# Performance work log

Hardware: AMD Instinct MI355X
Metric: run time of the kernel (lower is better)

Reference implementation:

```python
import jax, jax.numpy as jnp
import numpy as np

EPS = 1e-12  # torch F.normalize default eps


def _l2norm(x):
    n = jnp.sqrt(jnp.sum(x * x, axis=-1, keepdims=True))
    return x / jnp.maximum(n, EPS)


def setup_inputs() -> dict:
    key = jax.random.key(0)
    ks = jax.random.split(key, 8)
    B, T, V = 4, 2048, 512
    C, H, NB = 512, 4, 64
    return {
        "x": jax.random.normal(ks[0], (B, T, V), dtype=jnp.float32),
        "basis": jax.random.normal(ks[1], (V, 2 * NB), dtype=jnp.float32),
        "shared_q_w": jax.random.normal(ks[2], (V, C), dtype=jnp.float32) * 0.02,
        "shared_k_w": jax.random.normal(ks[3], (V, C), dtype=jnp.float32) * 0.02,
        "v_coeffs": jax.random.normal(ks[4], (C, 2 * NB), dtype=jnp.float32) * 0.02,
        "o_coeffs": jax.random.normal(ks[5], (C, 2 * NB), dtype=jnp.float32) * 0.02,
        "decay_logits": jnp.linspace(1.0, 5.0, H, dtype=jnp.float32),
        "out_scale": jnp.float32(0.1),
    }


def reference(x, basis, shared_q_w, shared_k_w, v_coeffs, o_coeffs, decay_logits, out_scale):
    B, T, V = x.shape
    H = decay_logits.shape[0]
    C = shared_q_w.shape[1]
    D = C // H

    v_w = basis @ v_coeffs.T  # [V, C]
    o_w = basis @ o_coeffs.T  # [V, C]

    q = _l2norm(x @ shared_q_w)  # [B, T, C]
    k = _l2norm(x @ shared_k_w)
    v = x @ v_w

    # [B, H, T, D]
    q = q.reshape(B, T, H, D).transpose(0, 2, 1, 3)
    k = k.reshape(B, T, H, D).transpose(0, 2, 1, 3)
    v = v.reshape(B, T, H, D).transpose(0, 2, 1, 3)

    scores = jnp.einsum("bhqd,bhkd->bhqk", q, k)  # [B, H, T, T]

    decay = jax.nn.sigmoid(decay_logits)  # [H]
    pos = jnp.arange(T)
    diff = pos[None, :] - pos[:, None]  # diff[i, j] = j - i
    mask = (diff > 0).astype(scores.dtype)  # [T, T]
    expo = jnp.clip(diff.astype(jnp.float32) - 1.0, 0.0, None)  # [T, T]
    decay_w = (decay[:, None, None] ** expo[None]) * mask[None]  # [H, T, T]

    scores = scores * decay_w[None].astype(scores.dtype)
    retrieved = jnp.einsum("bhqk,bhkd->bhqd", scores, v)  # [B, H, T, D]
    retrieved = retrieved.transpose(0, 2, 1, 3).reshape(B, T, C)
    return retrieved @ o_w.T * out_scale  # [B, T, V]
```

## Files before the change

### kernel.cpp

```cpp
#include <hip/hip_runtime.h>
#include <hip/hip_bf16.h>

#define BB 4
#define TT 2048
#define VV 512
#define CC 512
#define HH 4
#define DD 128
#define NB2 128
#define NROWS (BB*TT)
#define QC 64
#define NCH (TT/QC)
#define SST 66
#define EPS 1e-12f

typedef __attribute__((ext_vector_type(8))) short bf16x8;
typedef __attribute__((ext_vector_type(4))) float f32x4;
typedef unsigned short u16;

__device__ __forceinline__ void gl_lds16(const void* g, void* l) {
    __builtin_amdgcn_global_load_lds(
        (const __attribute__((address_space(1))) unsigned int*)g,
        (__attribute__((address_space(3))) unsigned int*)l, 16, 0, 0);
}
__device__ __forceinline__ u16 f2bu(float x) {
    __hip_bfloat16 h = __float2bfloat16(x);
    return *reinterpret_cast<u16*>(&h);
}
__device__ __forceinline__ float bu2f(u16 u) {
    __hip_bfloat16 h = *reinterpret_cast<__hip_bfloat16*>(&u);
    return __bfloat162float(h);
}
__device__ __forceinline__ uint4 pack8(float4 a, float4 b, float s) {
    u16 h[8] = {f2bu(a.x * s), f2bu(a.y * s), f2bu(a.z * s), f2bu(a.w * s),
                f2bu(b.x * s), f2bu(b.y * s), f2bu(b.z * s), f2bu(b.w * s)};
    return *(uint4*)h;
}

#define P2_CVT 4096
#define P2_TR  512
#define P2_Z   16
#define P2_WG  32
__global__ __launch_bounds__(256) void prep_all2(
    const float* __restrict__ x, const float* __restrict__ qw,
    const float* __restrict__ kw, const float* __restrict__ basis,
    const float* __restrict__ v_coeffs, const float* __restrict__ o_coeffs,
    const float* __restrict__ out_scale,
    u16* __restrict__ xb, u16* __restrict__ wq, u16* __restrict__ wk,
    u16* __restrict__ v_wT, u16* __restrict__ o_ws, float* __restrict__ norms)
{
    __shared__ __align__(16) union {
        float tile[32][33];
        struct { u16 A[4096]; u16 B[4096]; } w;
    } sm;
    const int bi = blockIdx.x, t = threadIdx.x;
    if (bi < P2_CVT) {
        int i = bi * 256 + t;
        float4 v = ((const float4*)x)[i];
        u16 h[4] = {f2bu(v.x), f2bu(v.y), f2bu(v.z), f2bu(v.w)};
        ((uint2*)xb)[i] = *(uint2*)h;
    } else if (bi < P2_CVT + P2_TR) {
        int id = bi - P2_CVT;
        const int z = id >> 8; id &= 255;
        const float* in = z ? kw : qw;
        u16* outT = z ? wk : wq;
        const int bx = (id & 15) * 32, by = (id >> 4) * 32;
        const int tx = t & 31, ty = t >> 5;
        #pragma unroll
        for (int r = 0; r < 32; r += 8)
            sm.tile[ty + r][tx] = in[(size_t)(by + ty + r) * CC + bx + tx];
        __syncthreads();
        #pragma unroll
        for (int r = 0; r < 32; r += 8)
            outT[(size_t)(bx + ty + r) * VV + by + tx] = f2bu(sm.tile[tx][ty + r]);
    } else if (bi < P2_CVT + P2_TR + P2_Z) {
        int idx = (bi - P2_CVT - P2_TR) * 256 + t;
        ((float4*)norms)[idx] = make_float4(0.f, 0.f, 0.f, 0.f);
    } else {
        int id = bi - (P2_CVT + P2_TR + P2_Z);
        const int sec = id >> 4, rem = id & 15;
        const int m0 = (rem >> 2) * 128, n0 = (rem & 3) * 128;
        const float* Af = sec ? basis : v_coeffs;
        const float* Bf = sec ? o_coeffs : basis;
        u16* Cp = sec ? o_ws : v_wT;
        const float scB = sec ? out_scale[0] : 1.f;
        const int wave = t >> 6, lane = t & 63;
        const int qq = lane >> 4, l16 = lane & 15;
        const int wm = (wave >> 1) * 64, wn = (wave & 1) * 64;
        const int s0 = wave * 128 + lane, s1 = s0 + 64;
        const int r0 = s0 >> 2, c0 = ((s0 & 3) - (r0 >> 1)) & 3;
        const int r1 = s1 >> 2, c1 = ((s1 & 3) - (r1 >> 1)) & 3;
        f32x4 acc[4][4];
        #pragma unroll
        for (int i = 0; i < 4; ++i)
            #pragma unroll
            for (int j = 0; j < 4; ++j) acc[i][j] = (f32x4){0.f, 0.f, 0.f, 0.f};
        for (int k0 = 0; k0 < NB2; k0 += 32) {
            __syncthreads();
            {
                const float* p0 = Af + (size_t)(m0 + r0) * NB2 + k0 + c0 * 8;
                const float* p1 = Af + (size_t)(m0 + r1) * NB2 + k0 + c1 * 8;
                *(uint4*)&sm.w.A[s0 * 8] = pack8(((const float4*)p0)[0], ((const float4*)p0)[1], 1.f);
                *(uint4*)&sm.w.A[s1 * 8] = pack8(((const float4*)p1)[0], ((const float4*)p1)[1], 1.f);
                const float* q0 = Bf + (size_t)(n0 + r0) * NB2 + k0 + c0 * 8;
                const float* q1 = Bf + (size_t)(n0 + r1) * NB2 + k0 + c1 * 8;
                *(uint4*)&sm.w.B[s0 * 8] = pack8(((const float4*)q0)[0], ((const float4*)q0)[1], scB);
                *(uint4*)&sm.w.B[s1 * 8] = pack8(((const float4*)q1)[0], ((const float4*)q1)[1], scB);
            }
            __syncthreads();
            bf16x8 af[4], bfr[4];
            #pragma unroll
            for (int mt = 0; mt < 4; ++mt) {
                const int r = wm + mt * 16 + l16;
                af[mt] = *(const bf16x8*)&sm.w.A[(r * 4 + ((qq + (r >> 1)) & 3)) * 8];
            }
            #pragma unroll
            for (int nt = 0; nt < 4; ++nt) {
                const int r = wn + nt * 16 + l16;
                bfr[nt] = *(const bf16x8*)&sm.w.B[(r * 4 + ((qq + (r >> 1)) & 3)) * 8];
            }
            #pragma unroll
            for (int mt = 0; mt < 4; ++mt)
                #pragma unroll
                for (int nt = 0; nt < 4; ++nt)
                    acc[mt][nt] = __builtin_amdgcn_mfma_f32_16x16x32_bf16(
                        af[mt], bfr[nt], acc[mt][nt], 0, 0, 0);
        }
        #pragma unroll
        for (int mt = 0; mt < 4; ++mt)
            #pragma unroll
            for (int rr = 0; rr < 4; ++rr) {
                int grow = m0 + wm + mt * 16 + qq * 4 + rr;
                #pragma unroll
                for (int nt = 0; nt < 4; ++nt)
                    Cp[(size_t)grow * 512 + n0 + wn + nt * 16 + l16] = f2bu(acc[mt][nt][rr]);
            }
    }
}

__global__ __launch_bounds__(256, 1) void gemm_qkv_fused(
    const u16* __restrict__ xb, const u16* __restrict__ wcat,
    u16* __restrict__ qo, u16* __restrict__ ko, u16* __restrict__ vo,
    float* __restrict__ norms)
{
    __shared__ __align__(16) u16 As[2 * 4096];
    __shared__ __align__(16) u16 Bs[3 * 2 * 4096];
    const int t = threadIdx.x;
    const int wave = t >> 6, lane = t & 63;
    const int qq = lane >> 4, l16 = lane & 15;
    const int m0 = blockIdx.y * 128, n0 = blockIdx.x * 128;
    const int wm = (wave >> 1) * 64, wn = (wave & 1) * 64;
    const int K = VV;

    const int s0 = wave * 128 + lane, s1 = s0 + 64;
    const int r0_ = s0 >> 2, c0_ = ((s0 & 3) - (r0_ >> 1)) & 3;
    const int r1_ = s1 >> 2, c1_ = ((s1 & 3) - (r1_ >> 1)) & 3;
    const u16* ga0 = xb + (size_t)(m0 + r0_) * K + c0_ * 8;
    const u16* ga1 = xb + (size_t)(m0 + r1_) * K + c1_ * 8;
    const u16* gb0[3];
    const u16* gb1[3];
    #pragma unroll
    for (int sec = 0; sec < 3; ++sec) {
        gb0[sec] = wcat + (size_t)sec * VV * CC + (size_t)(n0 + r0_) * K + c0_ * 8;
        gb1[sec] = wcat + (size_t)sec * VV * CC + (size_t)(n0 + r1_) * K + c1_ * 8;
    }
    const int lo0 = (wave * 128) * 8, lo1 = lo0 + 512;

    gl_lds16(ga0, As + lo0);
    gl_lds16(ga1, As + lo1);
    #pragma unroll
    for (int sec = 0; sec < 3; ++sec) {
        gl_lds16(gb0[sec], Bs + sec * 8192 + lo0);
        gl_lds16(gb1[sec], Bs + sec * 8192 + lo1);
    }

    f32x4 acc[3][4][4];
    #pragma unroll
    for (int s = 0; s < 3; ++s)
        #pragma unroll
        for (int i = 0; i < 4; ++i)
            #pragma unroll
            for (int j = 0; j < 4; ++j) acc[s][i][j] = (f32x4){0.f, 0.f, 0.f, 0.f};

    int ib = 0;
    for (int k0 = 0; k0 < K; k0 += 32, ib ^= 1) {
        __syncthreads();
        if (k0 + 32 < K) {
            const int off = (ib ^ 1) * 4096;
            gl_lds16(ga0 + k0 + 32, As + off + lo0);
            gl_lds16(ga1 + k0 + 32, As + off + lo1);
            #pragma unroll
            for (int sec = 0; sec < 3; ++sec) {
                gl_lds16(gb0[sec] + k0 + 32, Bs + sec * 8192 + off + lo0);
                gl_lds16(gb1[sec] + k0 + 32, Bs + sec * 8192 + off + lo1);
            }
        }
        const u16* Ac = As + ib * 4096;
        bf16x8 af[4];
        #pragma unroll
        for (int mt = 0; mt < 4; ++mt) {
            const int r = wm + mt * 16 + l16;
            af[mt] = *(const bf16x8*)&Ac[(r * 4 + ((qq + (r >> 1)) & 3)) * 8];
        }
        #pragma unroll
        for (int sec = 0; sec < 3; ++sec) {
            const u16* Bc = Bs + sec * 8192 + ib * 4096;
            bf16x8 bfr[4];
            #pragma unroll
            for (int nt = 0; nt < 4; ++nt) {
                const int r = wn + nt * 16 + l16;
                bfr[nt] = *(const bf16x8*)&Bc[(r * 4 + ((qq + (r >> 1)) & 3)) * 8];
            }
            #pragma unroll
            for (int mt = 0; mt < 4; ++mt)
                #pragma unroll
                for (int nt = 0; nt < 4; ++nt)
                    acc[sec][mt][nt] = __builtin_amdgcn_mfma_f32_16x16x32_bf16(
                        af[mt], bfr[nt], acc[sec][mt][nt], 0, 0, 0);
        }
    }
    #pragma unroll
    for (int sec = 0; sec < 3; ++sec) {
        u16* outp = sec == 0 ? qo : (sec == 1 ? ko : vo);
        #pragma unroll
        for (int mt = 0; mt < 4; ++mt)
            #pragma unroll
            for (int r = 0; r < 4; ++r) {
                int grow = m0 + wm + mt * 16 + qq * 4 + r;
                #pragma unroll
                for (int nt = 0; nt < 4; ++nt)
                    outp[(size_t)grow * CC + n0 + wn + nt * 16 + l16] =
                        f2bu(acc[sec][mt][nt][r]);
            }
        if (sec < 2) {
            float* np = sec == 0 ? norms : norms + NROWS;
            #pragma unroll
            for (int mt = 0; mt < 4; ++mt)
                #pragma unroll
                for (int r = 0; r < 4; ++r) {
                    float s = 0.f;
                    #pragma unroll
                    for (int nt = 0; nt < 4; ++nt) {
                        float v = acc[sec][mt][nt][r];
                        s = fmaf(v, v, s);
                    }
                    s += __shfl_xor(s, 1, 64);
                    s += __shfl_xor(s, 2, 64);
                    s += __shfl_xor(s, 4, 64);
                    s += __shfl_xor(s, 8, 64);
                    if (l16 == 0)
                        atomicAdd(&np[m0 + wm + mt * 16 + qq * 4 + r], s);
                }
        }
    }
}

__global__ __launch_bounds__(256) void state_local(
    const u16* __restrict__ kb, const u16* __restrict__ vb,
    const float* __restrict__ norms_k, const float* __restrict__ dlog,
    u16* __restrict__ statesb)
{
    __shared__ __align__(16) u16 vT[DD][SST];
    __shared__ __align__(16) u16 kT[DD][SST];
    const int c = blockIdx.x, bh = blockIdx.y;
    const int b = bh >> 2, h = bh & 3;
    const float lam = 1.f / (1.f + __expf(-dlog[h]));
    const float l2lam = log2f(lam);
    const int t = threadIdx.x;
    const int row0 = b * TT + c * QC;
    const size_t gbase = (size_t)row0 * CC + h * DD;

    {
        const int j2 = t & 31, d0 = (t >> 5) * 16;
        const int jj0 = 2 * j2, jj1 = jj0 + 1;
        const float w0 = exp2f((float)jj0 * l2lam);
        const float w1 = exp2f((float)jj1 * l2lam);
        const float rk0 = 1.f / fmaxf(sqrtf(norms_k[row0 + jj0]), EPS);
        const float rk1 = 1.f / fmaxf(sqrtf(norms_k[row0 + jj1]), EPS);
        u16 k0a[16], k1a[16], v0a[16], v1a[16];
        const u16* k0p = kb + gbase + (size_t)jj0 * CC + d0;
        const u16* k1p = kb + gbase + (size_t)jj1 * CC + d0;
        const u16* v0p = vb + gbase + (size_t)jj0 * CC + d0;
        const u16* v1p = vb + gbase + (size_t)jj1 * CC + d0;
        *(uint4*)&k0a[0] = *(const uint4*)k0p; *(uint4*)&k0a[8] = *(const uint4*)(k0p + 8);
        *(uint4*)&k1a[0] = *(const uint4*)k1p; *(uint4*)&k1a[8] = *(const uint4*)(k1p + 8);
        *(uint4*)&v0a[0] = *(const uint4*)v0p; *(uint4*)&v0a[8] = *(const uint4*)(v0p + 8);
        *(uint4*)&v1a[0] = *(const uint4*)v1p; *(uint4*)&v1a[8] = *(const uint4*)(v1p + 8);
        #pragma unroll
        for (int i = 0; i < 16; ++i) {
            unsigned int kw = (unsigned int)f2bu(bu2f(k0a[i]) * rk0)
                            | ((unsigned int)f2bu(bu2f(k1a[i]) * rk1) << 16);
            *(unsigned int*)&kT[d0 + i][jj0] = kw;
            unsigned int vw = (unsigned int)f2bu(bu2f(v0a[i]) * w0)
                            | ((unsigned int)f2bu(bu2f(v1a[i]) * w1) << 16);
            *(unsigned int*)&vT[d0 + i][jj0] = vw;
        }
    }
    __syncthreads();

    const int wave = t >> 6, lane = t & 63;
    const int quad = lane >> 4, l16 = lane & 15;
    f32x4 acc[2][8];
    #pragma unroll
    for (int i = 0; i < 2; ++i)
        #pragma unroll
        for (int j = 0; j < 8; ++j) acc[i][j] = (f32x4){0.f, 0.f, 0.f, 0.f};

    #pragma unroll
    for (int s = 0; s < 2; ++s) {
        bf16x8 af[2];
        #pragma unroll
        for (int mt = 0; mt < 2; ++mt)
            af[mt] = *(const bf16x8*)&vT[wave * 32 + mt * 16 + l16][s * 32 + quad * 8];
        #pragma unroll
        for (int nt = 0; nt < 8; ++nt) {
            bf16x8 bk = *(const bf16x8*)&kT[nt * 16 + l16][s * 32 + quad * 8];
            #pragma unroll
            for (int mt = 0; mt < 2; ++mt)
                acc[mt][nt] = __builtin_amdgcn_mfma_f32_16x16x32_bf16(
                    af[mt], bk, acc[mt][nt], 0, 0, 0);
        }
    }
    u16* so = statesb + ((size_t)(bh * NCH + c) << 14);
    #pragma unroll
    for (int mt = 0; mt < 2; ++mt)
        #pragma unroll
        for (int rr = 0; rr < 4; ++rr) {
            const int d = wave * 32 + mt * 16 + quad * 4 + rr;
            #pragma unroll
            for (int nt = 0; nt < 8; ++nt)
                so[(size_t)d * DD + nt * 16 + l16] = f2bu(acc[mt][nt][rr]);
        }
}

__global__ __launch_bounds__(256) void state_combine512(
    const float* __restrict__ dlog, u16* __restrict__ statesb)
{
    const int bh = blockIdx.x >> 5, part = blockIdx.x & 31;
    const int h = bh & 3;
    const float lam = 1.f / (1.f + __expf(-dlog[h]));
    const float lamQ = exp2f((float)QC * log2f(lam));
    const int t = threadIdx.x;
    unsigned int* pb = (unsigned int*)(statesb + ((size_t)(bh * NCH) << 14))
                       + part * 256 + t;
    float run0 = 0.f, run1 = 0.f;
    unsigned int cur = pb[(size_t)(NCH - 1) * 8192];
    for (int c = NCH - 1; c >= 0; --c) {
        unsigned int nxt = cur;
        if (c) nxt = pb[(size_t)(c - 1) * 8192];
        float t0 = bu2f((u16)(cur & 0xffffu));
        float t1 = bu2f((u16)(cur >> 16));
        pb[(size_t)c * 8192] = (unsigned int)f2bu(run0)
                             | ((unsigned int)f2bu(run1) << 16);
        run0 = fmaf(lamQ, run0, t0);
        run1 = fmaf(lamQ, run1, t1);
        cur = nxt;
    }
}

__global__ __launch_bounds__(256) void attention_fused(
    const u16* __restrict__ qb, const u16* __restrict__ kb,
    const u16* __restrict__ vb, const u16* __restrict__ statesb,
    const float* __restrict__ norms, const float* __restrict__ dlog,
    u16* __restrict__ retb)
{
    __shared__ __align__(16) u16 qks[2 * QC * DD];
    __shared__ __align__(16) u16 vsT[DD][SST];
    __shared__ __align__(16) u16 ss[QC][SST];
    __shared__ float rql[QC], rkl[QC];

    const int c = blockIdx.x, bh = blockIdx.y;
    const int b = bh >> 2, h = bh & 3;
    const float lam = 1.f / (1.f + __expf(-dlog[h]));
    const float l2lam = log2f(lam);
    const int t = threadIdx.x;
    const int row0 = b * TT + c * QC;
    const size_t base = (size_t)row0 * CC + h * DD;

    const int wave = t >> 6, lane = t & 63;
    const int quad = lane >> 4, l16 = lane & 15;
    const int r0 = wave * 16;

    {
        const int lrow = lane >> 4, cch = lane & 15;
        #pragma unroll
        for (int u = 0; u < 4; ++u) {
            const int R = wave * 16 + u * 4;
            const int gr = R + lrow;
            const int cq = (cch - gr) & 15;
            gl_lds16(qb + base + (size_t)gr * CC + cq * 8, &qks[R * DD]);
            gl_lds16(kb + base + (size_t)gr * CC + cq * 8, &qks[(QC + R) * DD]);
        }
    }
    if (t < QC)            rql[t]      = 1.f / fmaxf(sqrtf(norms[row0 + t]), EPS);
    else if (t < 2 * QC)   rkl[t - QC] = 1.f / fmaxf(sqrtf(norms[NROWS + row0 + t - QC]), EPS);
    {
        const int j2 = t & 31, d0 = (t >> 5) * 16;
        const u16* v0 = vb + base + (size_t)(2 * j2) * CC + d0;
        const u16* v1 = v0 + CC;
        uint4 a0 = *(const uint4*)v0;
        uint4 a1 = *(const uint4*)(v0 + 8);
        uint4 b0 = *(const uint4*)v1;
        uint4 b1 = *(const uint4*)(v1 + 8);
        const u16* ap0 = (const u16*)&a0; const u16* ap1 = (const u16*)&a1;
        const u16* bp0 = (const u16*)&b0; const u16* bp1 = (const u16*)&b1;
        #pragma unroll
        for (int i = 0; i < 8; ++i) {
            *(unsigned int*)&vsT[d0 + i][2 * j2] =
                (unsigned int)ap0[i] | ((unsigned int)bp0[i] << 16);
            *(unsigned int*)&vsT[d0 + 8 + i][2 * j2] =
                (unsigned int)ap1[i] | ((unsigned int)bp1[i] << 16);
        }
    }
    __syncthreads();

    bf16x8 aq[4];
    #pragma unroll
    for (int kq = 0; kq < 4; ++kq) {
        const int r = r0 + l16;
        aq[kq] = *(const bf16x8*)&qks[r * DD + ((kq * 4 + quad + r) & 15) * 8];
    }

    f32x4 accs[4];
    #pragma unroll
    for (int nt = 0; nt < 4; ++nt) accs[nt] = (f32x4){0.f, 0.f, 0.f, 0.f};
    #pragma unroll
    for (int nt = 0; nt < 4; ++nt)
        #pragma unroll
        for (int kq = 0; kq < 4; ++kq) {
            const int rk_ = nt * 16 + l16;
            bf16x8 bk = *(const bf16x8*)&qks[(QC + rk_) * DD + ((kq * 4 + quad + rk_) & 15) * 8];
            accs[nt] = __builtin_amdgcn_mfma_f32_16x16x32_bf16(aq[kq], bk, accs[nt], 0, 0, 0);
        }

    #pragma unroll
    for (int nt = 0; nt < 4; ++nt) {
        const int j = nt * 16 + l16;
        const float rkj = rkl[j];
        #pragma unroll
        for (int rr = 0; rr < 4; ++rr) {
            const int i = r0 + quad * 4 + rr;
            const int di = j - i;
            float p = (di > 0) ? accs[nt][rr] * exp2f((float)(di - 1) * l2lam) * rkj : 0.f;
            ss[i][j] = f2bu(p);
        }
    }
    __syncthreads();

    const u16* sb = statesb + ((size_t)(bh * NCH + c) << 14);
    {
        const int drow = lane >> 4, cch = lane & 15;
        #pragma unroll
        for (int u = 0; u < 8; ++u) {
            const int D = wave * 32 + u * 4;
            const int gd = D + drow;
            const int cq = (cch - gd) & 15;
            gl_lds16(sb + (size_t)gd * DD + cq * 8, &qks[D * DD]);
        }
    }
    bf16x8 ap[2];
    #pragma unroll
    for (int kj = 0; kj < 2; ++kj)
        ap[kj] = *(const bf16x8*)&ss[r0 + l16][kj * 32 + quad * 8];
    f32x4 accd[8];
    #pragma unroll
    for (int nt = 0; nt < 8; ++nt) accd[nt] = (f32x4){0.f, 0.f, 0.f, 0.f};
    #pragma unroll
    for (int nt = 0; nt < 8; ++nt)
        #pragma unroll
        for (int kj = 0; kj < 2; ++kj) {
            bf16x8 bv = *(const bf16x8*)&vsT[nt * 16 + l16][kj * 32 + quad * 8];
            accd[nt] = __builtin_amdgcn_mfma_f32_16x16x32_bf16(ap[kj], bv, accd[nt], 0, 0, 0);
        }
    __syncthreads();

    f32x4 accc[8];
    #pragma unroll
    for (int nt = 0; nt < 8; ++nt) accc[nt] = (f32x4){0.f, 0.f, 0.f, 0.f};
    #pragma unroll
    for (int nt = 0; nt < 8; ++nt)
        #pragma unroll
        for (int kq = 0; kq < 4; ++kq) {
            const int d = nt * 16 + l16;
            bf16x8 bs_ = *(const bf16x8*)&qks[d * DD + ((kq * 4 + quad + d) & 15) * 8];
            accc[nt] = __builtin_amdgcn_mfma_f32_16x16x32_bf16(aq[kq], bs_, accc[nt], 0, 0, 0);
        }

    u16* rb = retb + (size_t)row0 * CC + h * DD;
    #pragma unroll
    for (int rr = 0; rr < 4; ++rr) {
        const int ii = r0 + quad * 4 + rr;
        const float wrow = exp2f((float)(QC - 1 - ii) * l2lam);
        const float rq = rql[ii];
        #pragma unroll
        for (int nt = 0; nt < 8; ++nt) {
            float val = (accd[nt][rr] + wrow * accc[nt][rr]) * rq;
            rb[(size_t)ii * CC + nt * 16 + l16] = f2bu(val);
        }
    }
}

__global__ __launch_bounds__(256) void gemm_out64(
    const u16* __restrict__ A, const u16* __restrict__ Bt, float* __restrict__ C)
{
    __shared__ __align__(16) u16 As[4096];
    __shared__ __align__(16) u16 Bs[8192];
    const int t = threadIdx.x;
    const int wave = t >> 6, lane = t & 63;
    const int qq = lane >> 4, l16 = lane & 15;
    const int m0 = blockIdx.y * 64, n0 = blockIdx.x * 128;
    const int wm = (wave >> 1) * 32, wn = (wave & 1) * 64;
    const int N = VV, K = CC;

    const int sA = wave * 64 + lane;
    const int rA = sA >> 2, cA = ((sA & 3) - (rA >> 1)) & 3;
    const int sB0 = wave * 128 + lane, sB1 = sB0 + 64;
    const int rB0 = sB0 >> 2, cB0 = ((sB0 & 3) - (rB0 >> 1)) & 3;
    const int rB1 = sB1 >> 2, cB1 = ((sB1 & 3) - (rB1 >> 1)) & 3;
    const u16* ga  = A  + (size_t)(m0 + rA) * K + cA * 8;
    const u16* gb0 = Bt + (size_t)(n0 + rB0) * K + cB0 * 8;
    const u16* gb1 = Bt + (size_t)(n0 + rB1) * K + cB1 * 8;
    const int loA = wave * 512, loB0 = wave * 1024, loB1 = wave * 1024 + 512;

    gl_lds16(ga, As + loA);
    gl_lds16(gb0, Bs + loB0);
    gl_lds16(gb1, Bs + loB1);

    f32x4 acc[2][4];
    #pragma unroll
    for (int i = 0; i < 2; ++i)
        #pragma unroll
        for (int j = 0; j < 4; ++j) acc[i][j] = (f32x4){0.f, 0.f, 0.f, 0.f};

    int ib = 0;
    for (int k0 = 0; k0 < K; k0 += 32, ib ^= 1) {
        __syncthreads();
        if (k0 + 32 < K) {
            gl_lds16(ga + k0 + 32,  As + (ib ^ 1) * 2048 + loA);
            gl_lds16(gb0 + k0 + 32, Bs + (ib ^ 1) * 4096 + loB0);
            gl_lds16(gb1 + k0 + 32, Bs + (ib ^ 1) * 4096 + loB1);
        }
        const u16* Ac = As + ib * 2048;
        const u16* Bc = Bs + ib * 4096;
        bf16x8 af[2], bfr[4];
        #pragma unroll
        for (int mt = 0; mt < 2; ++mt) {
            const int r = wm + mt * 16 + l16;
            af[mt] = *(const bf16x8*)&Ac[(r * 4 + ((qq + (r >> 1)) & 3)) * 8];
        }
        #pragma unroll
        for (int nt = 0; nt < 4; ++nt) {
            const int r = wn + nt * 16 + l16;
            bfr[nt] = *(const bf16x8*)&Bc[(r * 4 + ((qq + (r >> 1)) & 3)) * 8];
        }
        #pragma unroll
        for (int mt = 0; mt < 2; ++mt)
            #pragma unroll
            for (int nt = 0; nt < 4; ++nt)
                acc[mt][nt] = __builtin_amdgcn_mfma_f32_16x16x32_bf16(
                    af[mt], bfr[nt], acc[mt][nt], 0, 0, 0);
    }
    #pragma unroll
    for (int mt = 0; mt < 2; ++mt)
        #pragma unroll
        for (int r = 0; r < 4; ++r) {
            int grow = m0 + wm + mt * 16 + qq * 4 + r;
            #pragma unroll
            for (int nt = 0; nt < 4; ++nt)
                C[(size_t)grow * N + n0 + wn + nt * 16 + l16] = acc[mt][nt][r];
        }
}

extern "C" void kernel_launch(void* const* d_in, const int* in_sizes, int n_in,
                              void* d_out, int out_size, void* d_ws, size_t ws_size,
                              hipStream_t stream) {
    const float* x         = (const float*)d_in[0];
    const float* basis     = (const float*)d_in[1];
    const float* qw        = (const float*)d_in[2];
    const float* kw        = (const float*)d_in[3];
    const float* v_coeffs  = (const float*)d_in[4];
    const float* o_coeffs  = (const float*)d_in[5];
    const float* dlog      = (const float*)d_in[6];
    const float* out_scale = (const float*)d_in[7];
    float* out             = (float*)d_out;

    u16* p = (u16*)d_ws;
    u16* qb      = p;
    u16* kb      = qb + (size_t)NROWS * CC;
    u16* vb      = kb + (size_t)NROWS * CC;
    u16* statesb = vb + (size_t)NROWS * CC;
    u16* xb      = statesb + (size_t)BB * HH * NCH * DD * DD;
    u16* retb    = xb;
    u16* wcat    = xb + (size_t)NROWS * CC;
    u16* o_ws    = wcat + 3 * (size_t)VV * CC;
    float* norms = (float*)(o_ws + (size_t)VV * CC);

    prep_all2<<<P2_CVT + P2_TR + P2_Z + P2_WG, 256, 0, stream>>>(
        x, qw, kw, basis, v_coeffs, o_coeffs, out_scale,
        xb, wcat, wcat + (size_t)VV * CC, wcat + 2 * (size_t)VV * CC, o_ws, norms);
    gemm_qkv_fused<<<dim3(4, NROWS / 128), 256, 0, stream>>>(xb, wcat, qb, kb, vb,
                                                             norms);
    state_local     <<<dim3(NCH, BB * HH), 256, 0, stream>>>(kb, vb, norms + NROWS,
                                                             dlog, statesb);
    state_combine512<<<BB * HH * 32, 256, 0, stream>>>(dlog, statesb);
    attention_fused <<<dim3(NCH, BB * HH), 256, 0, stream>>>(qb, kb, vb, statesb,
                                                             norms, dlog, retb);
    gemm_out64<<<dim3(VV / 128, NROWS / 64), 256, 0, stream>>>(retb, o_ws, out);
}
```

Measured before the change: 159.8 us.

## Fuse per-chunk state computation into QKV GEMM via last-block ticket

Removes the separate state_local launch. Each QKV GEMM block bumps an atomic ticket for its row tile, and the last of the four column blocks to finish computes the chunk states for that 128-row tile across all heads, reusing the GEMM's shared memory through a union. The state combine kernel also preloads all chunk values into registers before its sequential scan. This saves a launch and can overlap state work with other GEMM tiles, but it serialises 8 chunk-state computations inside one tail block and depends on the prep kernel zeroing the ticket counters (P2_Z is raised to 17).

```diff
diff --git a/kernel.cpp b/kernel.cpp
--- a/kernel.cpp
+++ b/kernel.cpp
@@ -39,7 +39,7 @@
 
 #define P2_CVT 4096
 #define P2_TR  512
-#define P2_Z   16
+#define P2_Z   17
 #define P2_WG  32
 __global__ __launch_bounds__(256) void prep_all2(
     const float* __restrict__ x, const float* __restrict__ qw,
@@ -141,10 +141,13 @@
 __global__ __launch_bounds__(256, 1) void gemm_qkv_fused(
     const u16* __restrict__ xb, const u16* __restrict__ wcat,
     u16* __restrict__ qo, u16* __restrict__ ko, u16* __restrict__ vo,
-    float* __restrict__ norms)
+    float* __restrict__ norms, const float* __restrict__ dlog,
+    u16* __restrict__ statesb, int* __restrict__ tickets)
 {
-    __shared__ __align__(16) u16 As[2 * 4096];
-    __shared__ __align__(16) u16 Bs[3 * 2 * 4096];
+    __shared__ __align__(16) union {
+        struct { u16 As[2 * 4096]; u16 Bs[3 * 2 * 4096]; } g;
+        struct { u16 vT[DD][SST]; u16 kT[DD][SST]; } s;
+    } sm;
     const int t = threadIdx.x;
     const int wave = t >> 6, lane = t & 63;
     const int qq = lane >> 4, l16 = lane & 15;
@@ -166,12 +169,12 @@
     }
     const int lo0 = (wave * 128) * 8, lo1 = lo0 + 512;
 
-    gl_lds16(ga0, As + lo0);
-    gl_lds16(ga1, As + lo1);
+    gl_lds16(ga0, sm.g.As + lo0);
+    gl_lds16(ga1, sm.g.As + lo1);
     #pragma unroll
     for (int sec = 0; sec < 3; ++sec) {
-        gl_lds16(gb0[sec], Bs + sec * 8192 + lo0);
-        gl_lds16(gb1[sec], Bs + sec * 8192 + lo1);
+        gl_lds16(gb0[sec], sm.g.Bs + sec * 8192 + lo0);
+        gl_lds16(gb1[sec], sm.g.Bs + sec * 8192 + lo1);
     }
 
     f32x4 acc[3][4][4];
@@ -187,15 +190,15 @@
         __syncthreads();
         if (k0 + 32 < K) {
             const int off = (ib ^ 1) * 4096;
-            gl_lds16(ga0 + k0 + 32, As + off + lo0);
-            gl_lds16(ga1 + k0 + 32, As + off + lo1);
+            gl_lds16(ga0 + k0 + 32, sm.g.As + off + lo0);
+            gl_lds16(ga1 + k0 + 32, sm.g.As + off + lo1);
             #pragma unroll
             for (int sec = 0; sec < 3; ++sec) {
-                gl_lds16(gb0[sec] + k0 + 32, Bs + sec * 8192 + off + lo0);
-                gl_lds16(gb1[sec] + k0 + 32, Bs + sec * 8192 + off + lo1);
-            }
-        }
-        const u16* Ac = As + ib * 4096;
+                gl_lds16(gb0[sec] + k0 + 32, sm.g.Bs + sec * 8192 + off + lo0);
+                gl_lds16(gb1[sec] + k0 + 32, sm.g.Bs + sec * 8192 + off + lo1);
+            }
+        }
+        const u16* Ac = sm.g.As + ib * 4096;
         bf16x8 af[4];
         #pragma unroll
         for (int mt = 0; mt < 4; ++mt) {
@@ -204,7 +207,7 @@
         }
         #pragma unroll
         for (int sec = 0; sec < 3; ++sec) {
-            const u16* Bc = Bs + sec * 8192 + ib * 4096;
+            const u16* Bc = sm.g.Bs + sec * 8192 + ib * 4096;
             bf16x8 bfr[4];
             #pragma unroll
             for (int nt = 0; nt < 4; ++nt) {
@@ -253,84 +256,85 @@
                 }
         }
     }
-}
-
-__global__ __launch_bounds__(256) void state_local(
-    const u16* __restrict__ kb, const u16* __restrict__ vb,
-    const float* __restrict__ norms_k, const float* __restrict__ dlog,
-    u16* __restrict__ statesb)
-{
-    __shared__ __align__(16) u16 vT[DD][SST];
-    __shared__ __align__(16) u16 kT[DD][SST];
-    const int c = blockIdx.x, bh = blockIdx.y;
-    const int b = bh >> 2, h = bh & 3;
-    const float lam = 1.f / (1.f + __expf(-dlog[h]));
-    const float l2lam = log2f(lam);
-    const int t = threadIdx.x;
-    const int row0 = b * TT + c * QC;
-    const size_t gbase = (size_t)row0 * CC + h * DD;
-
-    {
-        const int j2 = t & 31, d0 = (t >> 5) * 16;
-        const int jj0 = 2 * j2, jj1 = jj0 + 1;
-        const float w0 = exp2f((float)jj0 * l2lam);
-        const float w1 = exp2f((float)jj1 * l2lam);
-        const float rk0 = 1.f / fmaxf(sqrtf(norms_k[row0 + jj0]), EPS);
-        const float rk1 = 1.f / fmaxf(sqrtf(norms_k[row0 + jj1]), EPS);
-        u16 k0a[16], k1a[16], v0a[16], v1a[16];
-        const u16* k0p = kb + gbase + (size_t)jj0 * CC + d0;
-        const u16* k1p = kb + gbase + (size_t)jj1 * CC + d0;
-        const u16* v0p = vb + gbase + (size_t)jj0 * CC + d0;
-        const u16* v1p = vb + gbase + (size_t)jj1 * CC + d0;
-        *(uint4*)&k0a[0] = *(const uint4*)k0p; *(uint4*)&k0a[8] = *(const uint4*)(k0p + 8);
-        *(uint4*)&k1a[0] = *(const uint4*)k1p; *(uint4*)&k1a[8] = *(const uint4*)(k1p + 8);
-        *(uint4*)&v0a[0] = *(const uint4*)v0p; *(uint4*)&v0a[8] = *(const uint4*)(v0p + 8);
-        *(uint4*)&v1a[0] = *(const uint4*)v1p; *(uint4*)&v1a[8] = *(const uint4*)(v1p + 8);
-        #pragma unroll
-        for (int i = 0; i < 16; ++i) {
-            unsigned int kw = (unsigned int)f2bu(bu2f(k0a[i]) * rk0)
-                            | ((unsigned int)f2bu(bu2f(k1a[i]) * rk1) << 16);
-            *(unsigned int*)&kT[d0 + i][jj0] = kw;
-            unsigned int vw = (unsigned int)f2bu(bu2f(v0a[i]) * w0)
-                            | ((unsigned int)f2bu(bu2f(v1a[i]) * w1) << 16);
-            *(unsigned int*)&vT[d0 + i][jj0] = vw;
-        }
-    }
+
+    __threadfence();
     __syncthreads();
-
-    const int wave = t >> 6, lane = t & 63;
-    const int quad = lane >> 4, l16 = lane & 15;
-    f32x4 acc[2][8];
-    #pragma unroll
-    for (int i = 0; i < 2; ++i)
-        #pragma unroll
-        for (int j = 0; j < 8; ++j) acc[i][j] = (f32x4){0.f, 0.f, 0.f, 0.f};
-
-    #pragma unroll
-    for (int s = 0; s < 2; ++s) {
-        bf16x8 af[2];
-        #pragma unroll
-        for (int mt = 0; mt < 2; ++mt)
-            af[mt] = *(const bf16x8*)&vT[wave * 32 + mt * 16 + l16][s * 32 + quad * 8];
-        #pragma unroll
-        for (int nt = 0; nt < 8; ++nt) {
-            bf16x8 bk = *(const bf16x8*)&kT[nt * 16 + l16][s * 32 + quad * 8];
+    __shared__ int lastf;
+    if (t == 0) lastf = (atomicAdd(&tickets[blockIdx.y], 1) == 3);
+    __syncthreads();
+    if (!lastf) return;
+    __threadfence();
+
+    const int quad = qq;
+    const int b = m0 >> 11;
+    const int c0ch = (m0 & (TT - 1)) >> 6;
+    __syncthreads();
+    for (int h2 = 0; h2 < HH; ++h2) {
+        const float lam2 = 1.f / (1.f + __expf(-dlog[h2]));
+        const float l2l = log2f(lam2);
+        for (int ch = 0; ch < 2; ++ch) {
+            const int row0 = m0 + ch * QC;
+            const size_t gbase = (size_t)row0 * CC + h2 * DD;
+            u16* so = statesb + ((size_t)((b * HH + h2) * NCH + c0ch + ch) << 14);
+            {
+                const int j2 = t & 31, d0 = (t >> 5) * 16;
+                const int jj0 = 2 * j2, jj1 = jj0 + 1;
+                const float w0 = exp2f((float)jj0 * l2l);
+                const float w1 = exp2f((float)jj1 * l2l);
+                const float rk0 = 1.f / fmaxf(sqrtf(norms[NROWS + row0 + jj0]), EPS);
+                const float rk1 = 1.f / fmaxf(sqrtf(norms[NROWS + row0 + jj1]), EPS);
+                u16 k0a[16], k1a[16], v0a[16], v1a[16];
+                const u16* k0p = ko + gbase + (size_t)jj0 * CC + d0;
+                const u16* k1p = ko + gbase + (size_t)jj1 * CC + d0;
+                const u16* v0p = vo + gbase + (size_t)jj0 * CC + d0;
+                const u16* v1p = vo + gbase + (size_t)jj1 * CC + d0;
+                *(uint4*)&k0a[0] = *(const uint4*)k0p; *(uint4*)&k0a[8] = *(const uint4*)(k0p + 8);
+                *(uint4*)&k1a[0] = *(const uint4*)k1p; *(uint4*)&k1a[8] = *(const uint4*)(k1p + 8);
+                *(uint4*)&v0a[0] = *(const uint4*)v0p; *(uint4*)&v0a[8] = *(const uint4*)(v0p + 8);
+                *(uint4*)&v1a[0] = *(const uint4*)v1p; *(uint4*)&v1a[8] = *(const uint4*)(v1p + 8);
+                #pragma unroll
+                for (int i = 0; i < 16; ++i) {
+                    unsigned int kw = (unsigned int)f2bu(bu2f(k0a[i]) * rk0)
+                                    | ((unsigned int)f2bu(bu2f(k1a[i]) * rk1) << 16);
+                    *(unsigned int*)&sm.s.kT[d0 + i][jj0] = kw;
+                    unsigned int vw = (unsigned int)f2bu(bu2f(v0a[i]) * w0)
+                                    | ((unsigned int)f2bu(bu2f(v1a[i]) * w1) << 16);
+                    *(unsigned int*)&sm.s.vT[d0 + i][jj0] = vw;
+                }
+            }
+            __syncthreads();
+            f32x4 sacc[2][8];
+            #pragma unroll
+            for (int i = 0; i < 2; ++i)
+                #pragma unroll
+                for (int j = 0; j < 8; ++j) sacc[i][j] = (f32x4){0.f, 0.f, 0.f, 0.f};
+            #pragma unroll
+            for (int s = 0; s < 2; ++s) {
+                bf16x8 saf[2];
+                #pragma unroll
+                for (int mt = 0; mt < 2; ++mt)
+                    saf[mt] = *(const bf16x8*)&sm.s.vT[wave * 32 + mt * 16 + l16][s * 32 + quad * 8];
+                #pragma unroll
+                for (int nt = 0; nt < 8; ++nt) {
+                    bf16x8 bk = *(const bf16x8*)&sm.s.kT[nt * 16 + l16][s * 32 + quad * 8];
+                    #pragma unroll
+                    for (int mt = 0; mt < 2; ++mt)
+                        sacc[mt][nt] = __builtin_amdgcn_mfma_f32_16x16x32_bf16(
+                            saf[mt], bk, sacc[mt][nt], 0, 0, 0);
+                }
+            }
             #pragma unroll
             for (int mt = 0; mt < 2; ++mt)
-                acc[mt][nt] = __builtin_amdgcn_mfma_f32_16x16x32_bf16(
-                    af[mt], bk, acc[mt][nt], 0, 0, 0);
-        }
-    }
-    u16* so = statesb + ((size_t)(bh * NCH + c) << 14);
-    #pragma unroll
-    for (int mt = 0; mt < 2; ++mt)
-        #pragma unroll
-        for (int rr = 0; rr < 4; ++rr) {
-            const int d = wave * 32 + mt * 16 + quad * 4 + rr;
-            #pragma unroll
-            for (int nt = 0; nt < 8; ++nt)
-                so[(size_t)d * DD + nt * 16 + l16] = f2bu(acc[mt][nt][rr]);
-        }
+                #pragma unroll
+                for (int rr = 0; rr < 4; ++rr) {
+                    const int d = wave * 32 + mt * 16 + quad * 4 + rr;
+                    #pragma unroll
+                    for (int nt = 0; nt < 8; ++nt)
+                        so[(size_t)d * DD + nt * 16 + l16] = f2bu(sacc[mt][nt][rr]);
+                }
+            __syncthreads();
+        }
+    }
 }
 
 __global__ __launch_bounds__(256) void state_combine512(
@@ -343,18 +347,18 @@
     const int t = threadIdx.x;
     unsigned int* pb = (unsigned int*)(statesb + ((size_t)(bh * NCH) << 14))
                        + part * 256 + t;
+    unsigned int vals[NCH];
+    #pragma unroll
+    for (int c = 0; c < NCH; ++c) vals[c] = pb[(size_t)c * 8192];
     float run0 = 0.f, run1 = 0.f;
-    unsigned int cur = pb[(size_t)(NCH - 1) * 8192];
+    #pragma unroll
     for (int c = NCH - 1; c >= 0; --c) {
-        unsigned int nxt = cur;
-        if (c) nxt = pb[(size_t)(c - 1) * 8192];
-        float t0 = bu2f((u16)(cur & 0xffffu));
-        float t1 = bu2f((u16)(cur >> 16));
+        float t0 = bu2f((u16)(vals[c] & 0xffffu));
+        float t1 = bu2f((u16)(vals[c] >> 16));
         pb[(size_t)c * 8192] = (unsigned int)f2bu(run0)
                              | ((unsigned int)f2bu(run1) << 16);
         run0 = fmaf(lamQ, run0, t0);
         run1 = fmaf(lamQ, run1, t1);
-        cur = nxt;
     }
 }
 
@@ -594,14 +598,13 @@
     u16* wcat    = xb + (size_t)NROWS * CC;
     u16* o_ws    = wcat + 3 * (size_t)VV * CC;
     float* norms = (float*)(o_ws + (size_t)VV * CC);
+    int* tickets = (int*)(norms + 2 * NROWS);
 
     prep_all2<<<P2_CVT + P2_TR + P2_Z + P2_WG, 256, 0, stream>>>(
         x, qw, kw, basis, v_coeffs, o_coeffs, out_scale,
         xb, wcat, wcat + (size_t)VV * CC, wcat + 2 * (size_t)VV * CC, o_ws, norms);
-    gemm_qkv_fused<<<dim3(4, NROWS / 128), 256, 0, stream>>>(xb, wcat, qb, kb, vb,
-                                                             norms);
-    state_local     <<<dim3(NCH, BB * HH), 256, 0, stream>>>(kb, vb, norms + NROWS,
-                                                             dlog, statesb);
+    gemm_qkv_fused<<<dim3(4, NROWS / 128), 256, 0, stream>>>(
+        xb, wcat, qb, kb, vb, norms, dlog, statesb, tickets);
     state_combine512<<<BB * HH * 32, 256, 0, stream>>>(dlog, statesb);
     attention_fused <<<dim3(NCH, BB * HH), 256, 0, stream>>>(qb, kb, vb, statesb,
                                                              norms, dlog, retb);
```

Measured after the change: 218.3 us. 36.6% more time.

## Split fused QKV GEMM into per-section blocks and prefetch combine loads

Applied to the files above, without the earlier changes.

The fused QKV GEMM, where each block computed all three projections with three accumulator sets, becomes a kernel in which each block computes one projection. The grid triples to 12x64 blocks and LDS and register use per block drop, which allows more than one block per CU. In exchange, each A tile of x is now loaded three times instead of once. State_combine now loads all 32 chunk values up front into registers, instead of a one-ahead prefetch, so global load latency overlaps in the serial scan.

```diff
diff --git a/kernel.cpp b/kernel.cpp
--- a/kernel.cpp
+++ b/kernel.cpp
@@ -138,49 +138,42 @@
     }
 }
 
-__global__ __launch_bounds__(256, 1) void gemm_qkv_fused(
+__global__ __launch_bounds__(256) void gemm_qkv3(
     const u16* __restrict__ xb, const u16* __restrict__ wcat,
     u16* __restrict__ qo, u16* __restrict__ ko, u16* __restrict__ vo,
     float* __restrict__ norms)
 {
-    __shared__ __align__(16) u16 As[2 * 4096];
-    __shared__ __align__(16) u16 Bs[3 * 2 * 4096];
+    __shared__ __align__(16) u16 As[8192];
+    __shared__ __align__(16) u16 Bs[8192];
     const int t = threadIdx.x;
     const int wave = t >> 6, lane = t & 63;
     const int qq = lane >> 4, l16 = lane & 15;
-    const int m0 = blockIdx.y * 128, n0 = blockIdx.x * 128;
+    const int sec = blockIdx.x >> 2;
+    const int n0 = (blockIdx.x & 3) * 128;
+    const int m0 = blockIdx.y * 128;
     const int wm = (wave >> 1) * 64, wn = (wave & 1) * 64;
     const int K = VV;
+    const u16* Bt = wcat + (size_t)sec * VV * CC;
 
     const int s0 = wave * 128 + lane, s1 = s0 + 64;
     const int r0_ = s0 >> 2, c0_ = ((s0 & 3) - (r0_ >> 1)) & 3;
     const int r1_ = s1 >> 2, c1_ = ((s1 & 3) - (r1_ >> 1)) & 3;
     const u16* ga0 = xb + (size_t)(m0 + r0_) * K + c0_ * 8;
     const u16* ga1 = xb + (size_t)(m0 + r1_) * K + c1_ * 8;
-    const u16* gb0[3];
-    const u16* gb1[3];
-    #pragma unroll
-    for (int sec = 0; sec < 3; ++sec) {
-        gb0[sec] = wcat + (size_t)sec * VV * CC + (size_t)(n0 + r0_) * K + c0_ * 8;
-        gb1[sec] = wcat + (size_t)sec * VV * CC + (size_t)(n0 + r1_) * K + c1_ * 8;
-    }
+    const u16* gb0 = Bt + (size_t)(n0 + r0_) * K + c0_ * 8;
+    const u16* gb1 = Bt + (size_t)(n0 + r1_) * K + c1_ * 8;
     const int lo0 = (wave * 128) * 8, lo1 = lo0 + 512;
 
     gl_lds16(ga0, As + lo0);
     gl_lds16(ga1, As + lo1);
-    #pragma unroll
-    for (int sec = 0; sec < 3; ++sec) {
-        gl_lds16(gb0[sec], Bs + sec * 8192 + lo0);
-        gl_lds16(gb1[sec], Bs + sec * 8192 + lo1);
-    }
-
-    f32x4 acc[3][4][4];
-    #pragma unroll
-    for (int s = 0; s < 3; ++s)
-        #pragma unroll
-        for (int i = 0; i < 4; ++i)
-            #pragma unroll
-            for (int j = 0; j < 4; ++j) acc[s][i][j] = (f32x4){0.f, 0.f, 0.f, 0.f};
+    gl_lds16(gb0, Bs + lo0);
+    gl_lds16(gb1, Bs + lo1);
+
+    f32x4 acc[4][4];
+    #pragma unroll
+    for (int i = 0; i < 4; ++i)
+        #pragma unroll
+        for (int j = 0; j < 4; ++j) acc[i][j] = (f32x4){0.f, 0.f, 0.f, 0.f};
 
     int ib = 0;
     for (int k0 = 0; k0 < K; k0 += 32, ib ^= 1) {
@@ -189,69 +182,60 @@
             const int off = (ib ^ 1) * 4096;
             gl_lds16(ga0 + k0 + 32, As + off + lo0);
             gl_lds16(ga1 + k0 + 32, As + off + lo1);
-            #pragma unroll
-            for (int sec = 0; sec < 3; ++sec) {
-                gl_lds16(gb0[sec] + k0 + 32, Bs + sec * 8192 + off + lo0);
-                gl_lds16(gb1[sec] + k0 + 32, Bs + sec * 8192 + off + lo1);
-            }
+            gl_lds16(gb0 + k0 + 32, Bs + off + lo0);
+            gl_lds16(gb1 + k0 + 32, Bs + off + lo1);
         }
         const u16* Ac = As + ib * 4096;
-        bf16x8 af[4];
+        const u16* Bc = Bs + ib * 4096;
+        bf16x8 af[4], bfr[4];
         #pragma unroll
         for (int mt = 0; mt < 4; ++mt) {
             const int r = wm + mt * 16 + l16;
             af[mt] = *(const bf16x8*)&Ac[(r * 4 + ((qq + (r >> 1)) & 3)) * 8];
         }
         #pragma unroll
-        for (int sec = 0; sec < 3; ++sec) {
-            const u16* Bc = Bs + sec * 8192 + ib * 4096;
-            bf16x8 bfr[4];
-            #pragma unroll
-            for (int nt = 0; nt < 4; ++nt) {
-                const int r = wn + nt * 16 + l16;
-                bfr[nt] = *(const bf16x8*)&Bc[(r * 4 + ((qq + (r >> 1)) & 3)) * 8];
+        for (int nt = 0; nt < 4; ++nt) {
+            const int r = wn + nt * 16 + l16;
+            bfr[nt] = *(const bf16x8*)&Bc[(r * 4 + ((qq + (r >> 1)) & 3)) * 8];
+        }
+        #pragma unroll
+        for (int mt = 0; mt < 4; ++mt)
+            #pragma unroll
+            for (int nt = 0; nt < 4; ++nt)
+                acc[mt][nt] = __builtin_amdgcn_mfma_f32_16x16x32_bf16(
+                    af[mt], bfr[nt], acc[mt][nt], 0, 0, 0);
+    }
+
+    u16* outp = sec == 0 ? qo : (sec == 1 ? ko : vo);
+    #pragma unroll
+    for (int mt = 0; mt < 4; ++mt)
+        #pragma unroll
+        for (int r = 0; r < 4; ++r) {
+            int grow = m0 + wm + mt * 16 + qq * 4 + r;
+            #pragma unroll
+            for (int nt = 0; nt < 4; ++nt)
+                outp[(size_t)grow * CC + n0 + wn + nt * 16 + l16] =
+                    f2bu(acc[mt][nt][r]);
+        }
+    if (sec < 2) {
+        float* np = sec == 0 ? norms : norms + NROWS;
+        #pragma unroll
+        for (int mt = 0; mt < 4; ++mt)
+            #pragma unroll
+            for (int r = 0; r < 4; ++r) {
+                float s = 0.f;
+                #pragma unroll
+                for (int nt = 0; nt < 4; ++nt) {
+                    float v = acc[mt][nt][r];
+                    s = fmaf(v, v, s);
+                }
+                s += __shfl_xor(s, 1, 64);
+                s += __shfl_xor(s, 2, 64);
+                s += __shfl_xor(s, 4, 64);
+                s += __shfl_xor(s, 8, 64);
+                if (l16 == 0)
+                    atomicAdd(&np[m0 + wm + mt * 16 + qq * 4 + r], s);
             }
-            #pragma unroll
-            for (int mt = 0; mt < 4; ++mt)
-                #pragma unroll
-                for (int nt = 0; nt < 4; ++nt)
-                    acc[sec][mt][nt] = __builtin_amdgcn_mfma_f32_16x16x32_bf16(
-                        af[mt], bfr[nt], acc[sec][mt][nt], 0, 0, 0);
-        }
-    }
-    #pragma unroll
-    for (int sec = 0; sec < 3; ++sec) {
-        u16* outp = sec == 0 ? qo : (sec == 1 ? ko : vo);
-        #pragma unroll
-        for (int mt = 0; mt < 4; ++mt)
-            #pragma unroll
-            for (int r = 0; r < 4; ++r) {
-                int grow = m0 + wm + mt * 16 + qq * 4 + r;
-                #pragma unroll
-                for (int nt = 0; nt < 4; ++nt)
-                    outp[(size_t)grow * CC + n0 + wn + nt * 16 + l16] =
-                        f2bu(acc[sec][mt][nt][r]);
-            }
-        if (sec < 2) {
-            float* np = sec == 0 ? norms : norms + NROWS;
-            #pragma unroll
-            for (int mt = 0; mt < 4; ++mt)
-                #pragma unroll
-                for (int r = 0; r < 4; ++r) {
-                    float s = 0.f;
-                    #pragma unroll
-                    for (int nt = 0; nt < 4; ++nt) {
-                        float v = acc[sec][mt][nt][r];
-                        s = fmaf(v, v, s);
-                    }
-                    s += __shfl_xor(s, 1, 64);
-                    s += __shfl_xor(s, 2, 64);
-                    s += __shfl_xor(s, 4, 64);
-                    s += __shfl_xor(s, 8, 64);
-                    if (l16 == 0)
-                        atomicAdd(&np[m0 + wm + mt * 16 + qq * 4 + r], s);
-                }
-        }
     }
 }
 
@@ -343,18 +327,18 @@
     const int t = threadIdx.x;
     unsigned int* pb = (unsigned int*)(statesb + ((size_t)(bh * NCH) << 14))
                        + part * 256 + t;
+    unsigned int vals[NCH];
+    #pragma unroll
+    for (int c = 0; c < NCH; ++c) vals[c] = pb[(size_t)c * 8192];
     float run0 = 0.f, run1 = 0.f;
-    unsigned int cur = pb[(size_t)(NCH - 1) * 8192];
+    #pragma unroll
     for (int c = NCH - 1; c >= 0; --c) {
-        unsigned int nxt = cur;
-        if (c) nxt = pb[(size_t)(c - 1) * 8192];
-        float t0 = bu2f((u16)(cur & 0xffffu));
-        float t1 = bu2f((u16)(cur >> 16));
+        float t0 = bu2f((u16)(vals[c] & 0xffffu));
+        float t1 = bu2f((u16)(vals[c] >> 16));
         pb[(size_t)c * 8192] = (unsigned int)f2bu(run0)
                              | ((unsigned int)f2bu(run1) << 16);
         run0 = fmaf(lamQ, run0, t0);
         run1 = fmaf(lamQ, run1, t1);
-        cur = nxt;
     }
 }
 
@@ -598,8 +582,8 @@
     prep_all2<<<P2_CVT + P2_TR + P2_Z + P2_WG, 256, 0, stream>>>(
         x, qw, kw, basis, v_coeffs, o_coeffs, out_scale,
         xb, wcat, wcat + (size_t)VV * CC, wcat + 2 * (size_t)VV * CC, o_ws, norms);
-    gemm_qkv_fused<<<dim3(4, NROWS / 128), 256, 0, stream>>>(xb, wcat, qb, kb, vb,
-                                                             norms);
+    gemm_qkv3<<<dim3(12, NROWS / 128), 256, 0, stream>>>(xb, wcat, qb, kb, vb,
+                                                         norms);
     state_local     <<<dim3(NCH, BB * HH), 256, 0, stream>>>(kb, vb, norms + NROWS,
                                                              dlog, statesb);
     state_combine512<<<BB * HH * 32, 256, 0, stream>>>(dlog, statesb);
```

After: 160.9 us. About the same (+0.7%).
